# Kernel tuning notes

Measured on AMD Instinct MI355X. Metric: run time of the kernel, lower is better.

Reference implementation:

```python
import jax, jax.numpy as jnp
import numpy as np

B, T, I, H, O = 512, 512, 128, 512, 128


def setup_inputs() -> dict:
    key = jax.random.key(0)
    k = jax.random.split(key, 6)
    si = 1.0 / np.sqrt(I)
    sh = 1.0 / np.sqrt(H)
    x = jax.random.normal(k[0], (B, T, I), dtype=jnp.float32)
    # gate order along last axis: [g, i, f, o] (each H wide)
    Wx = jax.random.uniform(k[1], (I, 4 * H), jnp.float32, -si, si)
    Wh = jax.random.uniform(k[2], (H, 4 * H), jnp.float32, -sh, sh)
    b = jax.random.uniform(k[3], (4 * H,), jnp.float32, -sh, sh)
    Wp = jax.random.uniform(k[4], (H, O), jnp.float32, -sh, sh)
    bp = jax.random.uniform(k[5], (O,), jnp.float32, -sh, sh)
    return {"x": x, "Wx": Wx, "Wh": Wh, "b": b, "Wp": Wp, "bp": bp}


def reference(x, Wx, Wh, b, Wp, bp):
    # x: [B, T, I]. Fused LSTM: one input GEMM + one hidden GEMM per step,
    # gates split from the concatenated [g, i, f, o] projection.
    Bsz = x.shape[0]
    Hd = Wh.shape[0]
    # Precompute all input projections in one big GEMM: [T, B, 4H]
    xz = jnp.einsum('bti,ij->tbj', x, Wx)

    def step(carry, xzt):
        h, c = carry
        z = xzt + h @ Wh + b  # [B, 4H]
        g, i, f, o = jnp.split(z, 4, axis=-1)
        g = jnp.tanh(g)
        i = jax.nn.sigmoid(i)
        f = jax.nn.sigmoid(f)
        o = jax.nn.sigmoid(o)
        c = g * i + c * f
        h = jnp.tanh(c) * o
        return (h, c), None

    h0 = jnp.zeros((Bsz, Hd), dtype=x.dtype)
    c0 = jnp.zeros((Bsz, Hd), dtype=x.dtype)
    (h, c), _ = jax.lax.scan(step, (h0, c0), xz)
    p = h @ Wp + bp  # [B, O]
    return jax.nn.softmax(p, axis=1)
```

## Files before the change

kernel.cpp:

```cpp
#include <hip/hip_runtime.h>
#include <hip/hip_cooperative_groups.h>

namespace cg = cooperative_groups;

typedef _Float16 f16;
typedef _Float16 half8 __attribute__((ext_vector_type(8)));
typedef float float4v __attribute__((ext_vector_type(4)));
typedef unsigned long long u64;

constexpr int kB  = 512;
constexpr int kT  = 512;
constexpr int kI  = 128;
constexpr int kH  = 512;
constexpr int kNG = 2048;
constexpr int kO  = 128;

constexpr int LDK = 650;

__device__ __forceinline__ float fsig(float v)  { return 1.0f / (1.0f + __expf(-v)); }
__device__ __forceinline__ float ftanh(float v) { return 1.0f - 2.0f / (1.0f + __expf(2.0f * v)); }

union h8u { half8 h; u64 u[2]; };
union f16u { f16 f; unsigned short s; };

__global__ __launch_bounds__(256, 1) void lstm_fused(
    const float* __restrict__ x,  const float* __restrict__ Wx,
    const float* __restrict__ Wh, const float* __restrict__ bias,
    const float* __restrict__ Wp, const float* __restrict__ bp,
    float* __restrict__ out, float* __restrict__ ws)
{
  cg::grid_group grid = cg::this_grid();

  __shared__ __align__(16) f16 w_lds[64 * LDK];

  const int tid = threadIdx.x;
  const int wg  = blockIdx.x;
  const int bg  = wg & 7;
  const int ng  = wg >> 3;
  const int b0  = bg * 64;
  const int wv  = tid >> 6;
  const int l   = tid & 63;
  const int lc  = l & 15;
  const int lj  = l >> 4;

  f16* h16a = (f16*)ws;
  f16* h16b = h16a + kB * kH;
  unsigned* bar = (unsigned*)(h16b + kB * kH);

  {
    int gtid = wg * 256 + tid;
    unsigned* p = (unsigned*)h16a;
    p[gtid * 2] = 0u; p[gtid * 2 + 1] = 0u;
    if (gtid < 512) bar[gtid] = 0u;
  }

  for (int idx = tid; idx < 64 * 640; idx += 256) {
    int c = idx & 63;
    int k = idx >> 6;
    int gcol = (c >> 4) * 512 + ng * 16 + (c & 15);
    float v = (k < 512) ? Wh[(long)k * kNG + gcol]
                        : Wx[(long)(k - 512) * kNG + gcol];
    w_lds[c * LDK + k] = (f16)v;
  }
  float bb[4];
  #pragma unroll
  for (int g = 0; g < 4; ++g) bb[g] = bias[g * 512 + ng * 16 + lc];

  float ce[4] = {0.f, 0.f, 0.f, 0.f};
  const int arow = b0 + wv * 16 + lc;
  const f16* wbase = w_lds + lc * LDK + lj * 8;
  const float* xrow = x + (long)arow * (kT * kI) + lj * 8;

  grid.sync();

  unsigned* bcnt = bar + bg * 64;
  unsigned* bgen = bar + bg * 64 + 32;

  float4v xa[4], xb[4];
  #pragma unroll
  for (int q = 0; q < 4; ++q) {
    xa[q] = *(const float4v*)(xrow + q * 32);
    xb[q] = *(const float4v*)(xrow + q * 32 + 4);
  }

  for (int t = 0; t < kT; ++t) {
    const f16* hc = (t & 1) ? h16b : h16a;
    f16*       hn = (t & 1) ? h16a : h16b;

    const u64* hp64 = (const u64*)hc + (long)arow * 128 + lj * 2;
    h8u ah[16];
    #pragma unroll
    for (int p = 0; p < 16; ++p) {
      ah[p].u[0] = __hip_atomic_load(hp64 + p * 8,     __ATOMIC_RELAXED, __HIP_MEMORY_SCOPE_AGENT);
      ah[p].u[1] = __hip_atomic_load(hp64 + p * 8 + 1, __ATOMIC_RELAXED, __HIP_MEMORY_SCOPE_AGENT);
    }

    float4v acc[4];
    #pragma unroll
    for (int g = 0; g < 4; ++g) acc[g] = float4v{bb[g], bb[g], bb[g], bb[g]};

    #pragma unroll
    for (int ks = 0; ks < 16; ++ks) {
      #pragma unroll
      for (int g = 0; g < 4; ++g) {
        half8 bf = *(const half8*)(wbase + g * 16 * LDK + ks * 32);
        acc[g] = __builtin_amdgcn_mfma_f32_16x16x32_f16(ah[ks].h, bf, acc[g], 0, 0, 0);
      }
    }
    #pragma unroll
    for (int q = 0; q < 4; ++q) {
      half8 a;
      #pragma unroll
      for (int e = 0; e < 4; ++e) { a[e] = (f16)xa[q][e]; a[e + 4] = (f16)xb[q][e]; }
      #pragma unroll
      for (int g = 0; g < 4; ++g) {
        half8 bf = *(const half8*)(wbase + g * 16 * LDK + 512 + q * 32);
        acc[g] = __builtin_amdgcn_mfma_f32_16x16x32_f16(a, bf, acc[g], 0, 0, 0);
      }
    }

    if (t + 1 < kT) {
      const float* xn = xrow + (long)(t + 1) * kI;
      #pragma unroll
      for (int q = 0; q < 4; ++q) {
        xa[q] = *(const float4v*)(xn + q * 32);
        xb[q] = *(const float4v*)(xn + q * 32 + 4);
      }
    }

    #pragma unroll
    for (int e = 0; e < 4; ++e) {
      float gv = ftanh(acc[0][e]);
      float iv = fsig(acc[1][e]);
      float fv = fsig(acc[2][e]);
      float ov = fsig(acc[3][e]);
      float cn = gv * iv + ce[e] * fv;
      ce[e] = cn;
      f16u hv; hv.f = (f16)(ftanh(cn) * ov);
      unsigned short* dst = (unsigned short*)hn
          + (long)(b0 + wv * 16 + lj * 4 + e) * kH + ng * 16 + lc;
      __hip_atomic_store(dst, hv.s, __ATOMIC_RELAXED, __HIP_MEMORY_SCOPE_AGENT);
    }

    __syncthreads();
    if (tid == 0) {
      unsigned old = __hip_atomic_fetch_add(bcnt, 1u, __ATOMIC_RELAXED, __HIP_MEMORY_SCOPE_AGENT);
      if (old == (unsigned)(t * 32 + 31)) {
        __hip_atomic_store(bgen, (unsigned)(t + 1), __ATOMIC_RELAXED, __HIP_MEMORY_SCOPE_AGENT);
      } else {
        while (__hip_atomic_load(bgen, __ATOMIC_RELAXED, __HIP_MEMORY_SCOPE_AGENT) < (unsigned)(t + 1)) { }
      }
    }
    __syncthreads();
  }

  grid.sync();

  const f16* hf = h16a;
  float* hrow = (float*)w_lds;
  float* red  = (float*)w_lds + 2 * kH;
  for (int i = tid; i < 2 * kH; i += 256) {
    int r = i >> 9, k = i & 511;
    hrow[i] = (float)hf[(long)(wg * 2 + r) * kH + k];
  }
  __syncthreads();

  const int orow = tid >> 7;
  const int oc   = tid & 127;
  float p = bp[oc];
  #pragma unroll 8
  for (int k = 0; k < kH; ++k)
    p += hrow[orow * kH + k] * Wp[(long)k * kO + oc];

  red[tid] = p;
  __syncthreads();
  float m = -1e30f;
  for (int j = 0; j < 128; ++j) m = fmaxf(m, red[orow * 128 + j]);
  __syncthreads();
  float e = __expf(p - m);
  red[tid] = e;
  __syncthreads();
  float s = 0.f;
  for (int j = 0; j < 128; ++j) s += red[orow * 128 + j];
  out[(long)(wg * 2 + orow) * kO + oc] = e / s;
}

extern "C" void kernel_launch(void* const* d_in, const int* in_sizes, int n_in,
                              void* d_out, int out_size, void* d_ws, size_t ws_size,
                              hipStream_t stream) {
  const float* x  = (const float*)d_in[0];
  const float* Wx = (const float*)d_in[1];
  const float* Wh = (const float*)d_in[2];
  const float* b  = (const float*)d_in[3];
  const float* Wp = (const float*)d_in[4];
  const float* bp = (const float*)d_in[5];
  float* out = (float*)d_out;
  float* ws  = (float*)d_ws;

  void* args[] = { &x, &Wx, &Wh, &b, &Wp, &bp, &out, &ws };
  hipLaunchCooperativeKernel((void*)lstm_fused, dim3(256), dim3(256), args, 0, stream);
}
```

Before: 5.816 ms.

## Overlap next-step input projection with barrier wait and use per-block flag barrier

Moves the x-projection MFMAs for step t+1 (and the x prefetch for t+2) into the window between publishing this block's h and waiting on the group barrier, so the input GEMM is computed off the recurrence critical path. Replaces the single atomic counter plus generation flag with per-workgroup slots: each block stores its step number to its own slot and one wave polls all 32 slots of its batch group with a wave-wide all-vote. This removes the serialized fetch_add contention and one round trip, at the cost of more flag memory and more polling traffic.

```diff
diff --git a/kernel.cpp b/kernel.cpp
--- a/kernel.cpp
+++ b/kernel.cpp
@@ -51,7 +51,7 @@
     int gtid = wg * 256 + tid;
     unsigned* p = (unsigned*)h16a;
     p[gtid * 2] = 0u; p[gtid * 2 + 1] = 0u;
-    if (gtid < 512) bar[gtid] = 0u;
+    if (gtid < 8192) bar[gtid] = 0u;
   }
 
   for (int idx = tid; idx < 64 * 640; idx += 256) {
@@ -71,11 +71,6 @@
   const f16* wbase = w_lds + lc * LDK + lj * 8;
   const float* xrow = x + (long)arow * (kT * kI) + lj * 8;
 
-  grid.sync();
-
-  unsigned* bcnt = bar + bg * 64;
-  unsigned* bgen = bar + bg * 64 + 32;
-
   float4v xa[4], xb[4];
   #pragma unroll
   for (int q = 0; q < 4; ++q) {
@@ -83,6 +78,31 @@
     xb[q] = *(const float4v*)(xrow + q * 32 + 4);
   }
 
+  grid.sync();
+
+  unsigned* myslot = bar + (bg * 32 + ng) * 32;
+  const unsigned* pollslot = bar + (bg * 32 + (l & 31)) * 32;
+
+  float4v xacc[4];
+  #pragma unroll
+  for (int g = 0; g < 4; ++g) xacc[g] = float4v{bb[g], bb[g], bb[g], bb[g]};
+  #pragma unroll
+  for (int q = 0; q < 4; ++q) {
+    half8 a;
+    #pragma unroll
+    for (int e = 0; e < 4; ++e) { a[e] = (f16)xa[q][e]; a[e + 4] = (f16)xb[q][e]; }
+    #pragma unroll
+    for (int g = 0; g < 4; ++g) {
+      half8 bf = *(const half8*)(wbase + g * 16 * LDK + 512 + q * 32);
+      xacc[g] = __builtin_amdgcn_mfma_f32_16x16x32_f16(a, bf, xacc[g], 0, 0, 0);
+    }
+  }
+  #pragma unroll
+  for (int q = 0; q < 4; ++q) {
+    xa[q] = *(const float4v*)(xrow + kI + q * 32);
+    xb[q] = *(const float4v*)(xrow + kI + q * 32 + 4);
+  }
+
   for (int t = 0; t < kT; ++t) {
     const f16* hc = (t & 1) ? h16b : h16a;
     f16*       hn = (t & 1) ? h16a : h16b;
@@ -97,7 +117,7 @@
 
     float4v acc[4];
     #pragma unroll
-    for (int g = 0; g < 4; ++g) acc[g] = float4v{bb[g], bb[g], bb[g], bb[g]};
+    for (int g = 0; g < 4; ++g) acc[g] = xacc[g];
 
     #pragma unroll
     for (int ks = 0; ks < 16; ++ks) {
@@ -105,26 +125,6 @@
       for (int g = 0; g < 4; ++g) {
         half8 bf = *(const half8*)(wbase + g * 16 * LDK + ks * 32);
         acc[g] = __builtin_amdgcn_mfma_f32_16x16x32_f16(ah[ks].h, bf, acc[g], 0, 0, 0);
-      }
-    }
-    #pragma unroll
-    for (int q = 0; q < 4; ++q) {
-      half8 a;
-      #pragma unroll
-      for (int e = 0; e < 4; ++e) { a[e] = (f16)xa[q][e]; a[e + 4] = (f16)xb[q][e]; }
-      #pragma unroll
-      for (int g = 0; g < 4; ++g) {
-        half8 bf = *(const half8*)(wbase + g * 16 * LDK + 512 + q * 32);
-        acc[g] = __builtin_amdgcn_mfma_f32_16x16x32_f16(a, bf, acc[g], 0, 0, 0);
-      }
-    }
-
-    if (t + 1 < kT) {
-      const float* xn = xrow + (long)(t + 1) * kI;
-      #pragma unroll
-      for (int q = 0; q < 4; ++q) {
-        xa[q] = *(const float4v*)(xn + q * 32);
-        xb[q] = *(const float4v*)(xn + q * 32 + 4);
       }
     }
 
@@ -143,13 +143,38 @@
     }
 
     __syncthreads();
-    if (tid == 0) {
-      unsigned old = __hip_atomic_fetch_add(bcnt, 1u, __ATOMIC_RELAXED, __HIP_MEMORY_SCOPE_AGENT);
-      if (old == (unsigned)(t * 32 + 31)) {
-        __hip_atomic_store(bgen, (unsigned)(t + 1), __ATOMIC_RELAXED, __HIP_MEMORY_SCOPE_AGENT);
-      } else {
-        while (__hip_atomic_load(bgen, __ATOMIC_RELAXED, __HIP_MEMORY_SCOPE_AGENT) < (unsigned)(t + 1)) { }
+    if (tid == 0)
+      __hip_atomic_store(myslot, (unsigned)(t + 1), __ATOMIC_RELAXED, __HIP_MEMORY_SCOPE_AGENT);
+
+    if (t + 1 < kT) {
+      #pragma unroll
+      for (int g = 0; g < 4; ++g) xacc[g] = float4v{bb[g], bb[g], bb[g], bb[g]};
+      #pragma unroll
+      for (int q = 0; q < 4; ++q) {
+        half8 a;
+        #pragma unroll
+        for (int e = 0; e < 4; ++e) { a[e] = (f16)xa[q][e]; a[e + 4] = (f16)xb[q][e]; }
+        #pragma unroll
+        for (int g = 0; g < 4; ++g) {
+          half8 bf = *(const half8*)(wbase + g * 16 * LDK + 512 + q * 32);
+          xacc[g] = __builtin_amdgcn_mfma_f32_16x16x32_f16(a, bf, xacc[g], 0, 0, 0);
+        }
       }
+      if (t + 2 < kT) {
+        const float* xn = xrow + (long)(t + 2) * kI;
+        #pragma unroll
+        for (int q = 0; q < 4; ++q) {
+          xa[q] = *(const float4v*)(xn + q * 32);
+          xb[q] = *(const float4v*)(xn + q * 32 + 4);
+        }
+      }
+    }
+
+    if (wv == 0) {
+      unsigned v;
+      do {
+        v = __hip_atomic_load(pollslot, __ATOMIC_RELAXED, __HIP_MEMORY_SCOPE_AGENT);
+      } while (__all((int)(v >= (unsigned)(t + 1))) == 0);
     }
     __syncthreads();
   }
```

After: 5.558 ms. 1.05x faster.
